# Performance work log

Hardware: AMD Instinct MI355X
Metric: run time of the kernel (lower is better)

Reference implementation:

```python
import jax, jax.numpy as jnp
import numpy as np

B, S, H, NH, DH, I, C, P = 4, 1024, 1280, 20, 64, 5120, 13, 8
LN_EPS = 1e-5


def setup_inputs() -> dict:
    key = jax.random.key(0)
    ks = jax.random.split(key, 20)
    n = lambda k, shp, s=0.02: (jax.random.normal(k, shp, jnp.float32) * s)
    return {
        "hidden_states": jax.random.normal(ks[0], (B, S, H), jnp.float32),
        "attention_mask": jnp.ones((B, S), jnp.float32),
        "Wq": n(ks[1], (H, H)), "bq": jnp.zeros((H,), jnp.float32),
        "Wk": n(ks[2], (H, H)), "bk": jnp.zeros((H,), jnp.float32),
        "Wv": n(ks[3], (H, H)), "bv": jnp.zeros((H,), jnp.float32),
        "W_ct1": n(ks[4], (P, C), 0.3), "b_ct1": jnp.zeros((P,), jnp.float32),
        "W_ct2": n(ks[5], (P, C), 0.3), "b_ct2": jnp.zeros((P,), jnp.float32),
        "M": n(ks[6], (C, C), 0.5),
        "bias_scale": jnp.full((1,), 0.5, jnp.float32),
        "W_ptm": n(ks[7], (P, H)), "b_ptm": jnp.zeros((P,), jnp.float32),
        "ln_g": jnp.ones((H,), jnp.float32), "ln_b": jnp.zeros((H,), jnp.float32),
        "Wf1": n(ks[8], (I, H)), "bf1": jnp.zeros((I,), jnp.float32),
        "Wf2": n(ks[9], (H, I)), "bf2": jnp.zeros((H,), jnp.float32),
    }


def reference(hidden_states, attention_mask, Wq, bq, Wk, bk, Wv, bv,
              W_ct1, b_ct1, W_ct2, b_ct2, M, bias_scale, W_ptm, b_ptm,
              ln_g, ln_b, Wf1, bf1, Wf2, bf2):
    h = hidden_states
    # crosstalk bilinear projection: (P,C) @ (C,P) -> (P,P)
    out1 = (M.T @ W_ct1.T + b_ct1).T          # (P, C)
    out2 = M @ W_ct2.T + b_ct2                # (C, P)
    R = out1 @ out2                           # (P, P)
    # ptm_predictor (Linear H->P) + softmax
    ptm = jax.nn.softmax(h @ W_ptm.T + b_ptm, axis=-1)            # (B,S,P)
    Bb = jnp.tanh(jnp.einsum('blc,cd,bmd->blm', ptm, R, ptm)) * bias_scale  # (B,S,S)
    # manual multi-head attention
    q = (h @ Wq.T + bq).reshape(B, S, NH, DH).transpose(0, 2, 1, 3)
    k = (h @ Wk.T + bk).reshape(B, S, NH, DH).transpose(0, 2, 1, 3)
    v = (h @ Wv.T + bv).reshape(B, S, NH, DH).transpose(0, 2, 1, 3)
    scores = jnp.einsum('bhld,bhmd->bhlm', q, k) / np.float32(np.sqrt(DH))
    scores = scores + Bb[:, None]
    scores = scores + (1.0 - attention_mask)[:, None, None, :] * jnp.finfo(h.dtype).min
    probs = jax.nn.softmax(scores, axis=-1)
    ctx = jnp.einsum('bhlm,bhmd->bhld', probs, v)
    ctx = ctx.transpose(0, 2, 1, 3).reshape(B, S, H)
    # residual + LayerNorm
    x = h + ctx
    mu = jnp.mean(x, -1, keepdims=True)
    var = jnp.var(x, -1, keepdims=True)
    x = (x - mu) * jax.lax.rsqrt(var + LN_EPS) * ln_g + ln_b
    # FFN with exact GELU, residual
    ff = jax.nn.gelu(x @ Wf1.T + bf1, approximate=False) @ Wf2.T + bf2
    return x + ff
```

## Files before the change

kernel.cpp:

```cpp
#include <hip/hip_runtime.h>
#include <math.h>

typedef _Float16 f16;
typedef _Float16 f16x2 __attribute__((ext_vector_type(2)));
typedef _Float16 f16x8 __attribute__((ext_vector_type(8)));
typedef _Float16 f16x4 __attribute__((ext_vector_type(4)));
typedef float f32x4 __attribute__((ext_vector_type(4)));

#define B_ 4
#define S_ 1024
#define H_ 1280
#define NH_ 20
#define DH_ 64
#define I_ 5120
#define C_ 13
#define P_ 8
#define LOG2E 1.44269504088896f

__device__ __forceinline__ void store_val(float* p, float v) { *p = v; }
__device__ __forceinline__ void store_val(f16* p, float v) { *p = (f16)v; }

__global__ __launch_bounds__(256) void cvt6_kernel(
    const float* __restrict__ s0, f16* __restrict__ d0, int n0,
    const float* __restrict__ s1, f16* __restrict__ d1, int n1,
    const float* __restrict__ s2, f16* __restrict__ d2, int n2,
    const float* __restrict__ s3, f16* __restrict__ d3, int n3,
    const float* __restrict__ s4, f16* __restrict__ d4, int n4,
    const float* __restrict__ s5, f16* __restrict__ d5, int n5) {
    int seg = blockIdx.y;
    const float* src = (seg == 0) ? s0 : (seg == 1) ? s1 : (seg == 2) ? s2
                     : (seg == 3) ? s3 : (seg == 4) ? s4 : s5;
    f16* dst = (seg == 0) ? d0 : (seg == 1) ? d1 : (seg == 2) ? d2
             : (seg == 3) ? d3 : (seg == 4) ? d4 : d5;
    int n = (seg == 0) ? n0 : (seg == 1) ? n1 : (seg == 2) ? n2
          : (seg == 3) ? n3 : (seg == 4) ? n4 : n5;
    int i = blockIdx.x * 256 + threadIdx.x;
    if (i < n) {
        f32x4 v = ((const f32x4*)src)[i];
        f16x4 o;
#pragma unroll
        for (int e = 0; e < 4; e++) o[e] = (f16)v[e];
        ((f16x4*)dst)[i] = o;
    }
}

__global__ void crosstalk_kernel(const float* __restrict__ Mg,
                                 const float* __restrict__ W1, const float* __restrict__ b1,
                                 const float* __restrict__ W2, const float* __restrict__ b2,
                                 float* __restrict__ Rg) {
    __shared__ float o1[P_][C_];
    __shared__ float o2[C_][P_];
    int t = threadIdx.x;
    if (t < P_ * C_) {
        int p = t / C_, c = t % C_;
        float s = b1[p];
        for (int k = 0; k < C_; k++) s += Mg[k * C_ + c] * W1[p * C_ + k];
        o1[p][c] = s;
        int c2 = t / P_, p2 = t % P_;
        float s2 = b2[p2];
        for (int k = 0; k < C_; k++) s2 += Mg[c2 * C_ + k] * W2[p2 * C_ + k];
        o2[c2][p2] = s2;
    }
    __syncthreads();
    if (t < P_ * P_) {
        int p = t >> 3, q = t & 7;
        float s = 0.f;
        for (int c = 0; c < C_; c++) s += o1[p][c] * o2[c][q];
        Rg[t] = s;
    }
}

__global__ __launch_bounds__(256) void ptm_kernel(const float* __restrict__ hin,
                                                  const float* __restrict__ Wptm,
                                                  const float* __restrict__ bptm,
                                                  const float* __restrict__ Rg,
                                                  float* __restrict__ ptm,
                                                  float* __restrict__ tg) {
    int wv = threadIdx.x >> 6, lane = threadIdx.x & 63;
    int row = blockIdx.x * 4 + wv;
    const float* hrow = hin + (size_t)row * H_;
    float acc[P_] = {};
    for (int i = 0; i < H_ / 64; i++) {
        int k = lane + 64 * i;
        float hv = hrow[k];
#pragma unroll
        for (int p = 0; p < P_; p++) acc[p] += hv * Wptm[p * H_ + k];
    }
#pragma unroll
    for (int p = 0; p < P_; p++) {
#pragma unroll
        for (int o = 32; o >= 1; o >>= 1) acc[p] += __shfl_xor(acc[p], o);
        acc[p] += bptm[p];
    }
    float mx = acc[0];
#pragma unroll
    for (int p = 1; p < P_; p++) mx = fmaxf(mx, acc[p]);
    float sum = 0.f;
#pragma unroll
    for (int p = 0; p < P_; p++) { acc[p] = expf(acc[p] - mx); sum += acc[p]; }
    float rinv = 1.f / sum;
#pragma unroll
    for (int p = 0; p < P_; p++) acc[p] *= rinv;
    float tv[P_];
#pragma unroll
    for (int d = 0; d < P_; d++) {
        float s = 0.f;
#pragma unroll
        for (int c = 0; c < P_; c++) s += acc[c] * Rg[c * P_ + d];
        tv[d] = s;
    }
    if (lane == 0) {
#pragma unroll
        for (int p = 0; p < P_; p++) {
            ptm[(size_t)row * P_ + p] = acc[p];
            tg[(size_t)row * P_ + p]  = tv[p];
        }
    }
}

__global__ __launch_bounds__(256) void bias_kernel(const float* __restrict__ tg,
                                                   const float* __restrict__ ptm,
                                                   const float* __restrict__ mask,
                                                   const float* __restrict__ bscale_p,
                                                   f16* __restrict__ bb) {
    const int bl = blockIdx.x;
    const int b = bl >> 10;
    const int t = threadIdx.x;
    __shared__ float tl[P_];
    if (t < P_) tl[t] = tg[(size_t)bl * P_ + t];
    __syncthreads();
    const float bscale = bscale_p[0];
    float t0 = tl[0], t1 = tl[1], t2 = tl[2], t3 = tl[3];
    float t4 = tl[4], t5 = tl[5], t6 = tl[6], t7 = tl[7];
#pragma unroll
    for (int i = 0; i < 4; i++) {
        int m = t + 256 * i;
        const float* pm = ptm + ((size_t)b * S_ + m) * P_;
        float4 p0 = *(const float4*)pm;
        float4 p1 = *(const float4*)(pm + 4);
        float d = t0 * p0.x + t1 * p0.y + t2 * p0.z + t3 * p0.w
                + t4 * p1.x + t5 * p1.y + t6 * p1.z + t7 * p1.w;
        float v = (tanhf(d) * bscale + (1.0f - mask[(size_t)b * S_ + m]) * (-30000.0f)) * LOG2E;
        bb[(size_t)bl * S_ + m] = (f16)v;
    }
}

template <int MODE, typename YT>
__device__ __forceinline__ void gemm_body(const f16* __restrict__ X,
                                          const f16* __restrict__ W,
                                          const float* __restrict__ bias,
                                          YT* __restrict__ Y,
                                          const f16* __restrict__ res,
                                          int Ndim, int Kdim, int m0, int n0,
                                          f16* sA, f16* sB) {
    const int t = threadIdx.x;
    const int lane = t & 63, w = t >> 6;
    const int wr = w >> 1, wc = w & 1;
    const int lr = lane & 15, kq = lane >> 4;

    f32x4 acc[4][4] = {};

    int s_row[4], s_gc[4];
#pragma unroll
    for (int inst = 0; inst < 4; inst++) {
        int ci = t + 256 * inst;
        s_row[inst] = ci >> 3;
        s_gc[inst] = (ci & 7) ^ (s_row[inst] & 7);
    }

    for (int k0 = 0; k0 < Kdim; k0 += 64) {
        __syncthreads();
#pragma unroll
        for (int inst = 0; inst < 4; inst++) {
            int ci = t + 256 * inst;
            __builtin_amdgcn_global_load_lds(
                (const unsigned*)(X + (size_t)(m0 + s_row[inst]) * Kdim + k0 + s_gc[inst] * 8),
                (unsigned*)(sA + ci * 8), 16, 0, 0);
        }
#pragma unroll
        for (int inst = 0; inst < 4; inst++) {
            int ci = t + 256 * inst;
            __builtin_amdgcn_global_load_lds(
                (const unsigned*)(W + (size_t)(n0 + s_row[inst]) * Kdim + k0 + s_gc[inst] * 8),
                (unsigned*)(sB + ci * 8), 16, 0, 0);
        }
        __syncthreads();
#pragma unroll
        for (int ks = 0; ks < 2; ks++) {
            f16x8 af[4], bf[4];
#pragma unroll
            for (int i = 0; i < 4; i++) {
                int row = wr * 64 + i * 16 + lr;
                int cl = (ks * 4 + kq) ^ (row & 7);
                af[i] = *(const f16x8*)(sA + row * 64 + cl * 8);
            }
#pragma unroll
            for (int j = 0; j < 4; j++) {
                int row = wc * 64 + j * 16 + lr;
                int cl = (ks * 4 + kq) ^ (row & 7);
                bf[j] = *(const f16x8*)(sB + row * 64 + cl * 8);
            }
#pragma unroll
            for (int i = 0; i < 4; i++)
#pragma unroll
                for (int j = 0; j < 4; j++)
                    acc[i][j] = __builtin_amdgcn_mfma_f32_16x16x32_f16(af[i], bf[j], acc[i][j], 0, 0, 0);
        }
    }
#pragma unroll
    for (int j = 0; j < 4; j++) {
        int col = n0 + wc * 64 + j * 16 + lr;
        float bcol = bias[col];
#pragma unroll
        for (int i = 0; i < 4; i++) {
#pragma unroll
            for (int rr = 0; rr < 4; rr++) {
                int row = m0 + wr * 64 + i * 16 + kq * 4 + rr;
                float v = acc[i][j][rr] + bcol;
                if (MODE == 1) v = 0.5f * v * (1.0f + erff(v * 0.70710678118654752f));
                if (MODE == 2) v += (float)res[(size_t)row * Ndim + col];
                store_val(&Y[(size_t)row * Ndim + col], v);
            }
        }
    }
}

template <int MODE, typename YT>
__global__ __launch_bounds__(256, 2) void gemm128(const f16* __restrict__ X,
                                                  const f16* __restrict__ W,
                                                  const float* __restrict__ bias,
                                                  YT* __restrict__ Y,
                                                  const f16* __restrict__ res,
                                                  int Ndim, int Kdim) {
    __shared__ f16 sA[128 * 64];
    __shared__ f16 sB[128 * 64];
    gemm_body<MODE, YT>(X, W, bias, Y, res, Ndim, Kdim,
                        blockIdx.x * 128, blockIdx.y * 128, sA, sB);
}

__global__ __launch_bounds__(256, 2) void gemm_qkv(const f16* __restrict__ X,
                                                   const f16* __restrict__ Wq,
                                                   const f16* __restrict__ Wk,
                                                   const f16* __restrict__ Wv,
                                                   const float* __restrict__ bq,
                                                   const float* __restrict__ bk,
                                                   const float* __restrict__ bv,
                                                   f16* __restrict__ qb,
                                                   f16* __restrict__ kb,
                                                   f16* __restrict__ vb) {
    __shared__ f16 sA[128 * 64];
    __shared__ f16 sB[128 * 64];
    const int g = blockIdx.y / 10, nt = blockIdx.y % 10;
    const f16* W = (g == 0) ? Wq : (g == 1) ? Wk : Wv;
    const float* bias = (g == 0) ? bq : (g == 1) ? bk : bv;
    f16* Y = (g == 0) ? qb : (g == 1) ? kb : vb;
    gemm_body<0, f16>(X, W, bias, Y, nullptr, H_, H_,
                      blockIdx.x * 128, nt * 128, sA, sB);
}

__global__ __launch_bounds__(256) void attn_kernel(const f16* __restrict__ q,
                                                   const f16* __restrict__ k,
                                                   const f16* __restrict__ v,
                                                   const f16* __restrict__ bb,
                                                   const float* __restrict__ hin,
                                                   float* __restrict__ xpre) {
    __shared__ f16 sQ[64 * 72];
    __shared__ f16 sK[64 * 72];
    __shared__ f16 sVT[64 * 72];
    __shared__ f16 sP[64 * 72];

    const int t = threadIdx.x;
    const int w = t >> 6, lane = t & 63;
    const int lr = lane & 15, kq = lane >> 4;
    const int l0 = blockIdx.x * 64;
    const int h = blockIdx.y, b = blockIdx.z;
    const size_t base = (size_t)b * S_ * H_ + (size_t)h * DH_;

    for (int idx = t; idx < 512; idx += 256) {
        int r = idx >> 3, c8 = (idx & 7) * 8;
        f16x8 qv = *(const f16x8*)&q[base + (size_t)(l0 + r) * H_ + c8];
#pragma unroll
        for (int e = 0; e < 8; e++) qv[e] = (f16)((float)qv[e] * (0.125f * LOG2E));
        *(f16x8*)&sQ[r * 72 + c8] = qv;
    }
    __syncthreads();
    f16x8 afq[2];
    afq[0] = *(const f16x8*)&sQ[(w * 16 + lr) * 72 + kq * 8];
    afq[1] = *(const f16x8*)&sQ[(w * 16 + lr) * 72 + 32 + kq * 8];

    f32x4 acc_o[4] = {};
    float lstate[4] = {};

    const int vr2 = (t >> 3) * 2, vc8 = (t & 7) * 8;
    const int vmsw = vr2 ^ vc8;

    for (int mt = 0; mt < 16; mt++) {
        const int m0 = mt * 64;
        __syncthreads();
        for (int idx = t; idx < 512; idx += 256) {
            int r = idx >> 3, c8 = (idx & 7) * 8;
            f16x8 kvv = *(const f16x8*)&k[base + (size_t)(m0 + r) * H_ + c8];
            *(f16x8*)&sK[r * 72 + c8] = kvv;
        }
        {
            f16x8 v0 = *(const f16x8*)&v[base + (size_t)(m0 + vr2) * H_ + vc8];
            f16x8 v1 = *(const f16x8*)&v[base + (size_t)(m0 + vr2 + 1) * H_ + vc8];
#pragma unroll
            for (int e = 0; e < 8; e++) {
                f16x2 pk = {v0[e], v1[e]};
                *(f16x2*)&sVT[(vc8 + e) * 72 + vmsw] = pk;
            }
        }
        __syncthreads();

        f32x4 sacc[4] = {};
#pragma unroll
        for (int ks = 0; ks < 2; ks++)
#pragma unroll
            for (int j = 0; j < 4; j++) {
                f16x8 bk = *(const f16x8*)&sK[(j * 16 + lr) * 72 + ks * 32 + kq * 8];
                sacc[j] = __builtin_amdgcn_mfma_f32_16x16x32_f16(afq[ks], bk, sacc[j], 0, 0, 0);
            }
        const f16* bbrow = bb + ((size_t)b * S_ + l0 + w * 16 + kq * 4) * S_ + m0;
#pragma unroll
        for (int j = 0; j < 4; j++)
#pragma unroll
            for (int rr = 0; rr < 4; rr++)
                sacc[j][rr] += (float)bbrow[(size_t)rr * S_ + j * 16 + lr];

#pragma unroll
        for (int j = 0; j < 4; j++)
#pragma unroll
            for (int rr = 0; rr < 4; rr++) {
                float p = __builtin_exp2f(sacc[j][rr]);
                lstate[rr] += p;
                sP[(w * 16 + kq * 4 + rr) * 72 + j * 16 + lr] = (f16)p;
            }
        __syncthreads();

        f16x8 ap[2];
        ap[0] = *(const f16x8*)&sP[(w * 16 + lr) * 72 + kq * 8];
        ap[1] = *(const f16x8*)&sP[(w * 16 + lr) * 72 + 32 + kq * 8];
#pragma unroll
        for (int ks = 0; ks < 2; ks++)
#pragma unroll
            for (int j2 = 0; j2 < 4; j2++) {
                int d = j2 * 16 + lr;
                int s_ = (d >> 3) & 7;
                f16x8 bv = *(const f16x8*)&sVT[d * 72 + 8 * (((ks << 2) + kq) ^ s_)];
                acc_o[j2] = __builtin_amdgcn_mfma_f32_16x16x32_f16(ap[ks], bv, acc_o[j2], 0, 0, 0);
            }
    }

#pragma unroll
    for (int rr = 0; rr < 4; rr++) {
#pragma unroll
        for (int off = 8; off >= 1; off >>= 1) lstate[rr] += __shfl_xor(lstate[rr], off);
    }

#pragma unroll
    for (int rr = 0; rr < 4; rr++) {
        float linv = 1.0f / lstate[rr];
        int tok = l0 + w * 16 + kq * 4 + rr;
        size_t obase = base + (size_t)tok * H_;
#pragma unroll
        for (int j2 = 0; j2 < 4; j2++) {
            int d = j2 * 16 + lr;
            xpre[obase + d] = hin[obase + d] + acc_o[j2][rr] * linv;
        }
    }
}

__global__ __launch_bounds__(256) void ln_kernel(const float* __restrict__ xpre,
                                                 const float* __restrict__ g,
                                                 const float* __restrict__ bb,
                                                 f16* __restrict__ xln) {
    int row = blockIdx.x, t = threadIdx.x;
    const float* xr = xpre + (size_t)row * H_;
    float xv[5], s1 = 0.f, s2 = 0.f;
#pragma unroll
    for (int i = 0; i < 5; i++) {
        float v = xr[t + 256 * i];
        xv[i] = v; s1 += v; s2 += v * v;
    }
#pragma unroll
    for (int o = 32; o >= 1; o >>= 1) { s1 += __shfl_xor(s1, o); s2 += __shfl_xor(s2, o); }
    __shared__ float r1[4], r2[4];
    int wv = t >> 6, lane = t & 63;
    if (lane == 0) { r1[wv] = s1; r2[wv] = s2; }
    __syncthreads();
    float m1 = (r1[0] + r1[1] + r1[2] + r1[3]) * (1.0f / H_);
    float m2 = (r2[0] + r2[1] + r2[2] + r2[3]) * (1.0f / H_);
    float rstd = rsqrtf(m2 - m1 * m1 + 1e-5f);
#pragma unroll
    for (int i = 0; i < 5; i++) {
        int c = t + 256 * i;
        float v = (xv[i] - m1) * rstd * g[c] + bb[c];
        xln[(size_t)row * H_ + c] = (f16)v;
    }
}

extern "C" void kernel_launch(void* const* d_in, const int* in_sizes, int n_in,
                              void* d_out, int out_size, void* d_ws, size_t ws_size,
                              hipStream_t stream) {
    (void)in_sizes; (void)n_in; (void)out_size; (void)ws_size;
    const float* hin  = (const float*)d_in[0];
    const float* mask = (const float*)d_in[1];
    const float* Wq = (const float*)d_in[2];  const float* bq = (const float*)d_in[3];
    const float* Wk = (const float*)d_in[4];  const float* bk = (const float*)d_in[5];
    const float* Wv = (const float*)d_in[6];  const float* bv = (const float*)d_in[7];
    const float* Wct1 = (const float*)d_in[8];  const float* bct1 = (const float*)d_in[9];
    const float* Wct2 = (const float*)d_in[10]; const float* bct2 = (const float*)d_in[11];
    const float* Mg = (const float*)d_in[12];   const float* bscale = (const float*)d_in[13];
    const float* Wptm = (const float*)d_in[14]; const float* bptm = (const float*)d_in[15];
    const float* lng = (const float*)d_in[16];  const float* lnb = (const float*)d_in[17];
    const float* Wf1 = (const float*)d_in[18];  const float* bf1 = (const float*)d_in[19];
    const float* Wf2 = (const float*)d_in[20];  const float* bf2 = (const float*)d_in[21];

    char* ws = (char*)d_ws;
    const size_t SZ_PT  = (size_t)B_ * S_ * P_ * 4;
    const size_t SZ_H16 = (size_t)B_ * S_ * H_ * 2;
    const size_t SZ_H32 = (size_t)B_ * S_ * H_ * 4;
    const size_t SZ_WH  = (size_t)H_ * H_ * 2;
    const size_t SZ_WI  = (size_t)I_ * H_ * 2;
    float* Rg   = (float*)(ws);
    float* ptm  = (float*)(ws + 256);
    float* tg   = (float*)(ws + 256 + SZ_PT);
    char* A0    = ws + 256 + 2 * SZ_PT;
    f16* hin16  = (f16*)(A0);
    f16* qb     = (f16*)(A0 + SZ_H16);
    f16* kb     = (f16*)(A0 + 2 * SZ_H16);
    f16* vb     = (f16*)(A0 + 3 * SZ_H16);
    float* xpre = (float*)(A0 + 4 * SZ_H16);
    f16* xln    = (f16*)(A0 + 4 * SZ_H16 + SZ_H32);
    f16* bbias  = (f16*)(A0 + 5 * SZ_H16 + SZ_H32);
    char* WA    = A0 + 5 * SZ_H16 + SZ_H32 + (size_t)B_ * S_ * S_ * 2;
    f16* Wq16   = (f16*)(WA);
    f16* Wk16   = (f16*)(WA + SZ_WH);
    f16* Wv16   = (f16*)(WA + 2 * SZ_WH);
    f16* Wf116  = (f16*)(WA + 3 * SZ_WH);
    f16* Wf216  = (f16*)(WA + 3 * SZ_WH + SZ_WI);
    f16* g1     = (f16*)(A0);

    const int NH4 = (B_ * S_ * H_) / 4, NW4 = (H_ * H_) / 4, NI4 = (I_ * H_) / 4;
    cvt6_kernel<<<dim3((NI4 + 255) / 256, 6), 256, 0, stream>>>(
        hin, hin16, NH4, Wq, Wq16, NW4, Wk, Wk16, NW4,
        Wv, Wv16, NW4, Wf1, Wf116, NI4, Wf2, Wf216, NI4);

    crosstalk_kernel<<<1, 128, 0, stream>>>(Mg, Wct1, bct1, Wct2, bct2, Rg);
    ptm_kernel<<<S_ * B_ / 4, 256, 0, stream>>>(hin, Wptm, bptm, Rg, ptm, tg);
    bias_kernel<<<B_ * S_, 256, 0, stream>>>(tg, ptm, mask, bscale, bbias);
    gemm_qkv<<<dim3(32, 30), 256, 0, stream>>>(hin16, Wq16, Wk16, Wv16, bq, bk, bv, qb, kb, vb);
    attn_kernel<<<dim3(S_ / 64, NH_, B_), 256, 0, stream>>>(qb, kb, vb, bbias, hin, xpre);
    ln_kernel<<<B_ * S_, 256, 0, stream>>>(xpre, lng, lnb, xln);
    gemm128<1, f16><<<dim3(32, I_ / 128), 256, 0, stream>>>(xln, Wf116, bf1, g1, nullptr, I_, H_);
    gemm128<2, float><<<dim3(32, 10), 256, 0, stream>>>(g1, Wf216, bf2, (float*)d_out, xln, H_, I_);
}
```

Baseline: 494.3 us.

## Split-K the FFN down-projection GEMM and fold crosstalk into ptm kernel

The second FFN GEMM (K=5120) previously launched only 320 blocks. It now splits K in two across a grid z-dimension, so 640 blocks write fp32 partial outputs. A separate reduce kernel then adds the partials, bias and residual. This is meant to fill more of the GPU's compute units, at the cost of extra fp32 partial-buffer traffic and one more launch. Separately, each ptm block now recomputes the tiny crosstalk matrix R in shared memory, which removes a single-block kernel launch.

```diff
diff --git a/kernel.cpp b/kernel.cpp
--- a/kernel.cpp
+++ b/kernel.cpp
@@ -44,12 +44,19 @@
     }
 }
 
-__global__ void crosstalk_kernel(const float* __restrict__ Mg,
-                                 const float* __restrict__ W1, const float* __restrict__ b1,
-                                 const float* __restrict__ W2, const float* __restrict__ b2,
-                                 float* __restrict__ Rg) {
+__global__ __launch_bounds__(256) void ptm_kernel(const float* __restrict__ hin,
+                                                  const float* __restrict__ Wptm,
+                                                  const float* __restrict__ bptm,
+                                                  const float* __restrict__ Mg,
+                                                  const float* __restrict__ W1,
+                                                  const float* __restrict__ b1,
+                                                  const float* __restrict__ W2,
+                                                  const float* __restrict__ b2,
+                                                  float* __restrict__ ptm,
+                                                  float* __restrict__ tg) {
     __shared__ float o1[P_][C_];
     __shared__ float o2[C_][P_];
+    __shared__ float R[P_ * P_];
     int t = threadIdx.x;
     if (t < P_ * C_) {
         int p = t / C_, c = t % C_;
@@ -66,17 +73,11 @@
         int p = t >> 3, q = t & 7;
         float s = 0.f;
         for (int c = 0; c < C_; c++) s += o1[p][c] * o2[c][q];
-        Rg[t] = s;
-    }
-}
-
-__global__ __launch_bounds__(256) void ptm_kernel(const float* __restrict__ hin,
-                                                  const float* __restrict__ Wptm,
-                                                  const float* __restrict__ bptm,
-                                                  const float* __restrict__ Rg,
-                                                  float* __restrict__ ptm,
-                                                  float* __restrict__ tg) {
-    int wv = threadIdx.x >> 6, lane = threadIdx.x & 63;
+        R[t] = s;
+    }
+    __syncthreads();
+
+    int wv = t >> 6, lane = t & 63;
     int row = blockIdx.x * 4 + wv;
     const float* hrow = hin + (size_t)row * H_;
     float acc[P_] = {};
@@ -106,7 +107,7 @@
     for (int d = 0; d < P_; d++) {
         float s = 0.f;
 #pragma unroll
-        for (int c = 0; c < P_; c++) s += acc[c] * Rg[c * P_ + d];
+        for (int c = 0; c < P_; c++) s += acc[c] * R[c * P_ + d];
         tv[d] = s;
     }
     if (lane == 0) {
@@ -151,8 +152,8 @@
                                           const float* __restrict__ bias,
                                           YT* __restrict__ Y,
                                           const f16* __restrict__ res,
-                                          int Ndim, int Kdim, int m0, int n0,
-                                          f16* sA, f16* sB) {
+                                          int Ndim, int Kdim, int kbeg, int kend,
+                                          int m0, int n0, f16* sA, f16* sB) {
     const int t = threadIdx.x;
     const int lane = t & 63, w = t >> 6;
     const int wr = w >> 1, wc = w & 1;
@@ -168,7 +169,7 @@
         s_gc[inst] = (ci & 7) ^ (s_row[inst] & 7);
     }
 
-    for (int k0 = 0; k0 < Kdim; k0 += 64) {
+    for (int k0 = kbeg; k0 < kend; k0 += 64) {
         __syncthreads();
 #pragma unroll
         for (int inst = 0; inst < 4; inst++) {
@@ -210,7 +211,7 @@
 #pragma unroll
     for (int j = 0; j < 4; j++) {
         int col = n0 + wc * 64 + j * 16 + lr;
-        float bcol = bias[col];
+        float bcol = (MODE == 3) ? 0.f : bias[col];
 #pragma unroll
         for (int i = 0; i < 4; i++) {
 #pragma unroll
@@ -234,8 +235,38 @@
                                                   int Ndim, int Kdim) {
     __shared__ f16 sA[128 * 64];
     __shared__ f16 sB[128 * 64];
-    gemm_body<MODE, YT>(X, W, bias, Y, res, Ndim, Kdim,
+    gemm_body<MODE, YT>(X, W, bias, Y, res, Ndim, Kdim, 0, Kdim,
                         blockIdx.x * 128, blockIdx.y * 128, sA, sB);
+}
+
+__global__ __launch_bounds__(256, 2) void gemm_sk(const f16* __restrict__ X,
+                                                  const f16* __restrict__ W,
+                                                  float* __restrict__ Pb,
+                                                  int Ndim, int Kdim, int Mdim) {
+    __shared__ f16 sA[128 * 64];
+    __shared__ f16 sB[128 * 64];
+    const int kd2 = Kdim >> 1;
+    float* Y = Pb + (size_t)blockIdx.z * Mdim * Ndim;
+    gemm_body<3, float>(X, W, nullptr, Y, nullptr, Ndim, Kdim,
+                        blockIdx.z * kd2, blockIdx.z * kd2 + kd2,
+                        blockIdx.x * 128, blockIdx.y * 128, sA, sB);
+}
+
+__global__ __launch_bounds__(256) void reduce2_kernel(const float* __restrict__ p0,
+                                                      const float* __restrict__ p1,
+                                                      const float* __restrict__ bias,
+                                                      const f16* __restrict__ res,
+                                                      float* __restrict__ out) {
+    int i = blockIdx.x * 256 + threadIdx.x;
+    int col = (i * 4) % H_;
+    f32x4 a = ((const f32x4*)p0)[i];
+    f32x4 b = ((const f32x4*)p1)[i];
+    f32x4 bc = *(const f32x4*)(bias + col);
+    f16x4 r = ((const f16x4*)res)[i];
+    f32x4 o;
+#pragma unroll
+    for (int e = 0; e < 4; e++) o[e] = a[e] + b[e] + bc[e] + (float)r[e];
+    ((f32x4*)out)[i] = o;
 }
 
 __global__ __launch_bounds__(256, 2) void gemm_qkv(const f16* __restrict__ X,
@@ -254,7 +285,7 @@
     const f16* W = (g == 0) ? Wq : (g == 1) ? Wk : Wv;
     const float* bias = (g == 0) ? bq : (g == 1) ? bk : bv;
     f16* Y = (g == 0) ? qb : (g == 1) ? kb : vb;
-    gemm_body<0, f16>(X, W, bias, Y, nullptr, H_, H_,
+    gemm_body<0, f16>(X, W, bias, Y, nullptr, H_, H_, 0, H_,
                       blockIdx.x * 128, nt * 128, sA, sB);
 }
 
@@ -423,7 +454,6 @@
     const size_t SZ_H32 = (size_t)B_ * S_ * H_ * 4;
     const size_t SZ_WH  = (size_t)H_ * H_ * 2;
     const size_t SZ_WI  = (size_t)I_ * H_ * 2;
-    float* Rg   = (float*)(ws);
     float* ptm  = (float*)(ws + 256);
     float* tg   = (float*)(ws + 256 + SZ_PT);
     char* A0    = ws + 256 + 2 * SZ_PT;
@@ -441,18 +471,21 @@
     f16* Wf116  = (f16*)(WA + 3 * SZ_WH);
     f16* Wf216  = (f16*)(WA + 3 * SZ_WH + SZ_WI);
     f16* g1     = (f16*)(A0);
+    float* pbuf = (float*)(WA + 3 * SZ_WH + 2 * SZ_WI);
 
     const int NH4 = (B_ * S_ * H_) / 4, NW4 = (H_ * H_) / 4, NI4 = (I_ * H_) / 4;
     cvt6_kernel<<<dim3((NI4 + 255) / 256, 6), 256, 0, stream>>>(
         hin, hin16, NH4, Wq, Wq16, NW4, Wk, Wk16, NW4,
         Wv, Wv16, NW4, Wf1, Wf116, NI4, Wf2, Wf216, NI4);
 
-    crosstalk_kernel<<<1, 128, 0, stream>>>(Mg, Wct1, bct1, Wct2, bct2, Rg);
-    ptm_kernel<<<S_ * B_ / 4, 256, 0, stream>>>(hin, Wptm, bptm, Rg, ptm, tg);
+    ptm_kernel<<<S_ * B_ / 4, 256, 0, stream>>>(hin, Wptm, bptm,
+                                                Mg, Wct1, bct1, Wct2, bct2, ptm, tg);
     bias_kernel<<<B_ * S_, 256, 0, stream>>>(tg, ptm, mask, bscale, bbias);
     gemm_qkv<<<dim3(32, 30), 256, 0, stream>>>(hin16, Wq16, Wk16, Wv16, bq, bk, bv, qb, kb, vb);
     attn_kernel<<<dim3(S_ / 64, NH_, B_), 256, 0, stream>>>(qb, kb, vb, bbias, hin, xpre);
     ln_kernel<<<B_ * S_, 256, 0, stream>>>(xpre, lng, lnb, xln);
     gemm128<1, f16><<<dim3(32, I_ / 128), 256, 0, stream>>>(xln, Wf116, bf1, g1, nullptr, I_, H_);
-    gemm128<2, float><<<dim3(32, 10), 256, 0, stream>>>(g1, Wf216, bf2, (float*)d_out, xln, H_, I_);
-}
+    gemm_sk<<<dim3(32, 10, 2), 256, 0, stream>>>(g1, Wf216, pbuf, H_, I_, B_ * S_);
+    reduce2_kernel<<<(B_ * S_ * H_) / 4 / 256, 256, 0, stream>>>(
+        pbuf, pbuf + (size_t)B_ * S_ * H_, bf2, xln, (float*)d_out);
+}
```

New measurement: 465.7 us. 5.8% less time.
